# Kernel tuning notes

Measured on AMD Instinct MI355X. Metric: run time of the kernel, lower is better.

Reference implementation:

```python
import jax, jax.numpy as jnp
import numpy as np

EPS = 0.5          # residual scaling (module __init__ eps)
N = 100_000        # num nodes
E = 1_250_000      # num edges (avg degree ~12.5)
D = 64             # feature dim


def setup_inputs() -> dict:
    key = jax.random.key(0)
    k1, k2, k3 = jax.random.split(key, 3)
    x = jax.random.normal(k1, (N, D), dtype=jnp.float32)
    src = jax.random.randint(k2, (E,), 0, N, dtype=jnp.int32)
    dst = jax.random.randint(k3, (E,), 0, N, dtype=jnp.int32)
    return {"x": x, "src": src, "dst": dst}


def reference(x, src, dst):
    n = x.shape[0]
    # out-degree of each node = number of edges with that node as source
    deg = jax.ops.segment_sum(jnp.ones(src.shape, dtype=x.dtype), src, num_segments=n)
    norm = jnp.power(jnp.maximum(deg, 1.0), -0.5)          # [N]
    edge_norm = norm[src] * norm[dst]                      # [E] (u_mul_v)
    msg = x[src] * edge_norm[:, None]                      # [E, D] (u_mul_e)
    h = jax.ops.segment_sum(msg, dst, num_segments=n)      # sum per destination
    return h + x * EPS
```

## Files before the change

### kernel.cpp

```cpp
#include <hip/hip_runtime.h>

constexpr int D        = 64;
constexpr float EPS    = 0.5f;
constexpr int BKT      = 256;
constexpr int CAPB_MAX = 4096;
constexpr int EPB      = 4096;
constexpr int PTHREADS = 512;
constexpr int EPT      = EPB / PTHREADS;
constexpr int GTHREADS = 1024;
constexpr int NTHREADS = 512;
constexpr int NBMAX    = 512;
constexpr int MAXOVF   = 65536;

__device__ __forceinline__ unsigned int f2bf(float f) {
    unsigned int u = __float_as_uint(f);
    return (u + 0x7FFFu + ((u >> 16) & 1u)) >> 16;
}
__device__ __forceinline__ float bf2f_lo(unsigned int v) { return __uint_as_float(v << 16); }
__device__ __forceinline__ float bf2f_hi(unsigned int v) { return __uint_as_float(v & 0xFFFF0000u); }


__global__ __launch_bounds__(PTHREADS)
void partition_kernel(const int* __restrict__ src, const int* __restrict__ dst,
                      int* __restrict__ curD, int* __restrict__ curS,
                      unsigned int* __restrict__ rec, unsigned char* __restrict__ srec,
                      int* __restrict__ ovf_cnt, int* __restrict__ ovf,
                      int* __restrict__ sovf_cnt, int* __restrict__ sovf,
                      int E, int NB, int capb) {
    __shared__ int histD[NBMAX];
    __shared__ int histS[NBMAX];
    __shared__ int startD[NBMAX];
    __shared__ int startS[NBMAX];
    const int base = blockIdx.x * EPB;
    const int tid  = threadIdx.x;
    const bool full = (base + EPB) <= E;
    for (int b = tid; b < NB; b += PTHREADS) { histD[b] = 0; histS[b] = 0; }
    __syncthreads();

    if (full) {
        const int4* s4 = (const int4*)(src + base);
        const int4* d4 = (const int4*)(dst + base);
        #pragma unroll
        for (int k = 0; k < EPT / 4; ++k) {
            int4 sv = s4[tid + k * PTHREADS];
            int4 dv = d4[tid + k * PTHREADS];
            atomicAdd(&histD[dv.x >> 8], 1); atomicAdd(&histS[sv.x >> 8], 1);
            atomicAdd(&histD[dv.y >> 8], 1); atomicAdd(&histS[sv.y >> 8], 1);
            atomicAdd(&histD[dv.z >> 8], 1); atomicAdd(&histS[sv.z >> 8], 1);
            atomicAdd(&histD[dv.w >> 8], 1); atomicAdd(&histS[sv.w >> 8], 1);
        }
    } else {
        for (int k = 0; k < EPT; ++k) {
            int e = base + tid + k * PTHREADS;
            if (e < E) {
                atomicAdd(&histD[dst[e] >> 8], 1);
                atomicAdd(&histS[src[e] >> 8], 1);
            }
        }
    }
    __syncthreads();
    for (int b = tid; b < NB; b += PTHREADS) {
        int c = histD[b];
        startD[b] = (c > 0) ? atomicAdd(&curD[b], c) : 0;
        histD[b] = 0;
        int c2 = histS[b];
        startS[b] = (c2 > 0) ? atomicAdd(&curS[b], c2) : 0;
        histS[b] = 0;
    }
    __syncthreads();
    if (full) {
        const int4* s4 = (const int4*)(src + base);
        const int4* d4 = (const int4*)(dst + base);
        #pragma unroll
        for (int k = 0; k < EPT / 4; ++k) {
            int4 sv = s4[tid + k * PTHREADS];
            int4 dv = d4[tid + k * PTHREADS];
            int ss[4] = {sv.x, sv.y, sv.z, sv.w};
            int tt[4] = {dv.x, dv.y, dv.z, dv.w};
            #pragma unroll
            for (int j = 0; j < 4; ++j) {
                int s = ss[j], t = tt[j];
                int bD = t >> 8;
                int r  = atomicAdd(&histD[bD], 1);
                int p  = startD[bD] + r;
                if (p < capb) {
                    rec[(size_t)bD * capb + p] = ((unsigned int)s << 8) | (unsigned int)(t & (BKT - 1));
                } else {
                    int i = atomicAdd(ovf_cnt, 1);
                    if (i < MAXOVF) { ovf[2 * i] = s; ovf[2 * i + 1] = t; }
                }
                int bS = s >> 8;
                int r2 = atomicAdd(&histS[bS], 1);
                int p2 = startS[bS] + r2;
                if (p2 < capb) {
                    srec[(size_t)bS * capb + p2] = (unsigned char)(s & (BKT - 1));
                } else {
                    int i = atomicAdd(sovf_cnt, 1);
                    if (i < MAXOVF) sovf[i] = s;
                }
            }
        }
    } else {
        for (int k = 0; k < EPT; ++k) {
            int e = base + tid + k * PTHREADS;
            if (e < E) {
                int s = src[e], t = dst[e];
                int bD = t >> 8;
                int r  = atomicAdd(&histD[bD], 1);
                int p  = startD[bD] + r;
                if (p < capb) {
                    rec[(size_t)bD * capb + p] = ((unsigned int)s << 8) | (unsigned int)(t & (BKT - 1));
                } else {
                    int i = atomicAdd(ovf_cnt, 1);
                    if (i < MAXOVF) { ovf[2 * i] = s; ovf[2 * i + 1] = t; }
                }
                int bS = s >> 8;
                int r2 = atomicAdd(&histS[bS], 1);
                int p2 = startS[bS] + r2;
                if (p2 < capb) {
                    srec[(size_t)bS * capb + p2] = (unsigned char)(s & (BKT - 1));
                } else {
                    int i = atomicAdd(sovf_cnt, 1);
                    if (i < MAXOVF) sovf[i] = s;
                }
            }
        }
    }
}

__global__ __launch_bounds__(NTHREADS)
void degnorm_kernel(const unsigned char* __restrict__ srec, const int* __restrict__ curS,
                    const int* __restrict__ sovf_cnt, const int* __restrict__ sovf,
                    float* __restrict__ norm, int n, int capb) {
    const int b   = blockIdx.x;
    const int tid = threadIdx.x;
    __shared__ int hist[BKT];
    if (tid < BKT) hist[tid] = 0;
    __syncthreads();
    int cnt = curS[b];
    if (cnt > capb) cnt = capb;
    const unsigned int* s4 = (const unsigned int*)(srec + (size_t)b * capb);
    int nw = cnt >> 2;
    for (int i = tid; i < nw; i += NTHREADS) {
        unsigned int w = s4[i];
        atomicAdd(&hist[w & 255u], 1);
        atomicAdd(&hist[(w >> 8) & 255u], 1);
        atomicAdd(&hist[(w >> 16) & 255u], 1);
        atomicAdd(&hist[w >> 24], 1);
    }
    for (int i = (nw << 2) + tid; i < cnt; i += NTHREADS)
        atomicAdd(&hist[srec[(size_t)b * capb + i]], 1);
    int oc = *sovf_cnt;
    if (oc > 0) {
        if (oc > MAXOVF) oc = MAXOVF;
        for (int i = tid; i < oc; i += NTHREADS) {
            int s = sovf[i];
            if ((s >> 8) == b) atomicAdd(&hist[s & (BKT - 1)], 1);
        }
    }
    __syncthreads();
    if (tid < BKT) {
        int node = b * BKT + tid;
        if (node < n) norm[node] = rsqrtf(fmaxf((float)hist[tid], 1.0f));
    }
}

__global__ __launch_bounds__(256)
void yhconv_kernel(const float2* __restrict__ x2, const float* __restrict__ norm,
                   unsigned int* __restrict__ yh, int total) {
    int stride = gridDim.x * 256;
    for (int i = blockIdx.x * 256 + threadIdx.x; i < total; i += stride) {
        float2 v = x2[i];
        float nm = norm[i >> 5];
        yh[i] = f2bf(v.x * nm) | (f2bf(v.y * nm) << 16);
    }
}

__global__ __launch_bounds__(GTHREADS)
void sortgather_kernel(const unsigned int* __restrict__ rec, const int* __restrict__ curD,
                       const float* __restrict__ norm, const uint4* __restrict__ yr4,
                       const float4* __restrict__ x4, float4* __restrict__ out4,
                       int n, int capb) {
    __shared__ unsigned int recs[CAPB_MAX];
    __shared__ unsigned int srcs[CAPB_MAX];
    __shared__ int hist[BKT];
    __shared__ int rankb[BKT];
    __shared__ int rsL[BKT];
    __shared__ float nrmL[BKT];
    __shared__ unsigned int wsums[GTHREADS / 64];
    const int b   = blockIdx.x;
    const int tid = threadIdx.x;
    const int lane = tid & 63;
    const int wid  = tid >> 6;

    int cnt = curD[b];
    if (cnt > capb) cnt = capb;
    for (int i = tid; i < cnt; i += GTHREADS) recs[i] = rec[(size_t)b * capb + i];
    if (tid < BKT) {
        hist[tid] = 0;
        int node = b * BKT + tid;
        nrmL[tid] = (node < n) ? norm[node] : 1.0f;
    }
    __syncthreads();
    for (int i = tid; i < cnt; i += GTHREADS) atomicAdd(&hist[recs[i] & (BKT - 1)], 1);
    __syncthreads();
    {
        int v = (tid < BKT) ? hist[tid] : 0;
        #pragma unroll
        for (int off = 1; off < 64; off <<= 1) {
            int t = __shfl_up(v, off);
            if (lane >= off) v += t;
        }
        if (tid < BKT && lane == 63) wsums[wid] = (unsigned int)v;
        __syncthreads();
        if (tid < BKT) {
            int add = 0;
            #pragma unroll
            for (int w = 0; w < BKT / 64; ++w)
                if (w < wid) add += (int)wsums[w];
            int excl = v + add - hist[tid];
            rankb[tid] = excl;
            rsL[tid]   = excl;
        }
    }
    __syncthreads();
    for (int i = tid; i < cnt; i += GTHREADS) {
        unsigned int v = recs[i];
        int pos = atomicAdd(&rankb[v & (BKT - 1)], 1);
        srcs[pos] = v >> 8;
    }
    __syncthreads();

    const int fl  = lane & 7;
    const int oct = lane >> 3;
    #pragma unroll
    for (int r = 0; r < BKT / 128; ++r) {
        int ln   = r * 128 + wid * 8 + oct;
        int node = b * BKT + ln;
        bool valid = node < n;
        int rsl = valid ? rsL[ln]  : 0;
        int cl  = valid ? hist[ln] : 0;
        int m = cl;
        m = max(m, __shfl_xor(m, 8));
        m = max(m, __shfl_xor(m, 16));
        m = max(m, __shfl_xor(m, 32));
        float a0 = 0.f, a1 = 0.f, a2 = 0.f, a3 = 0.f;
        float a4 = 0.f, a5 = 0.f, a6 = 0.f, a7 = 0.f;
        for (int k = 0; k < m; k += 8) {
            int sb[8];
            #pragma unroll
            for (int j = 0; j < 8; ++j) {
                int kj = k + j;
                sb[j] = (kj < cl) ? (int)srcs[rsl + kj] : -1;
            }
            #pragma unroll
            for (int j = 0; j < 8; ++j) {
                bool take = sb[j] >= 0;
                int s = take ? sb[j] : 0;
                uint4 v = yr4[(size_t)s * 8 + fl];
                if (!take) { v.x = 0u; v.y = 0u; v.z = 0u; v.w = 0u; }
                a0 += bf2f_lo(v.x); a1 += bf2f_hi(v.x);
                a2 += bf2f_lo(v.y); a3 += bf2f_hi(v.y);
                a4 += bf2f_lo(v.z); a5 += bf2f_hi(v.z);
                a6 += bf2f_lo(v.w); a7 += bf2f_hi(v.w);
            }
        }
        if (valid) {
            float nt = nrmL[ln];
            size_t basei = (size_t)node * 16 + fl * 2;
            float4 xv0 = x4[basei], xv1 = x4[basei + 1];
            float4 r0, r1;
            r0.x = a0 * nt + EPS * xv0.x;  r0.y = a1 * nt + EPS * xv0.y;
            r0.z = a2 * nt + EPS * xv0.z;  r0.w = a3 * nt + EPS * xv0.w;
            r1.x = a4 * nt + EPS * xv1.x;  r1.y = a5 * nt + EPS * xv1.y;
            r1.z = a6 * nt + EPS * xv1.z;  r1.w = a7 * nt + EPS * xv1.w;
            out4[basei] = r0;
            out4[basei + 1] = r1;
        }
    }
}

__global__ void cleanup_kernel(const float* __restrict__ x, const float* __restrict__ norm,
                               const int* __restrict__ ovf_cnt, const int* __restrict__ ovf,
                               float* __restrict__ out) {
    int cnt = *ovf_cnt;
    if (cnt > MAXOVF) cnt = MAXOVF;
    long long total = (long long)cnt * D;
    long long stride = (long long)gridDim.x * blockDim.x;
    for (long long i = blockIdx.x * (long long)blockDim.x + threadIdx.x; i < total; i += stride) {
        int e = (int)(i >> 6), d = (int)(i & 63);
        int s = ovf[2 * e], t = ovf[2 * e + 1];
        atomicAdd(&out[(size_t)t * D + d], norm[s] * norm[t] * x[(size_t)s * D + d]);
    }
}


__global__ void fb_hist(const int* __restrict__ src, int* __restrict__ deg, int E) {
    int e = blockIdx.x * blockDim.x + threadIdx.x;
    if (e < E) atomicAdd(&deg[src[e]], 1);
}
__global__ void fb_norm(const int* __restrict__ deg, float* __restrict__ norm, int n) {
    int i = blockIdx.x * blockDim.x + threadIdx.x;
    if (i < n) norm[i] = rsqrtf(fmaxf((float)deg[i], 1.0f));
}
__global__ void fb_init_out(const float4* __restrict__ x, float4* __restrict__ out, int n4) {
    int i = blockIdx.x * blockDim.x + threadIdx.x;
    if (i < n4) {
        float4 v = x[i];
        out[i] = make_float4(v.x * EPS, v.y * EPS, v.z * EPS, v.w * EPS);
    }
}
__global__ void fb_scatter(const float* __restrict__ x, const int* __restrict__ src,
                           const int* __restrict__ dst, const float* __restrict__ norm,
                           float* __restrict__ out, int E) {
    long long tid = (long long)blockIdx.x * blockDim.x + threadIdx.x;
    int e = (int)(tid >> 6), d = (int)(tid & 63);
    if (e < E) {
        int s = src[e], t = dst[e];
        atomicAdd(&out[(size_t)t * D + d], norm[s] * norm[t] * x[(size_t)s * D + d]);
    }
}


extern "C" void kernel_launch(void* const* d_in, const int* in_sizes, int n_in,
                              void* d_out, int out_size, void* d_ws, size_t ws_size,
                              hipStream_t stream) {
    const float* x   = (const float*)d_in[0];
    const int*   src = (const int*)d_in[1];
    const int*   dst = (const int*)d_in[2];
    float* out = (float*)d_out;

    const int ND = in_sizes[0];
    const int E  = in_sizes[1];
    const int n  = ND / D;
    const int NB = (n + BKT - 1) / BKT;
    constexpr int B = 256;
    const int NB64 = (NB + 63) & ~63;

    int capb = 0;
    for (int c : {4096, 3584}) {
        size_t srecB = ((size_t)NB * c + 15) & ~15ull;
        size_t need = (size_t)NB * c * 4
                    + srecB
                    + (size_t)ND * 2
                    + (size_t)n * 4
                    + (size_t)(2 * NB64 + 128) * 4
                    + (size_t)3 * MAXOVF * 4;
        if (need <= ws_size) { capb = c; break; }
    }

    if (NB <= NBMAX && capb > 0 && n < (1 << 24) && E > 0) {
        unsigned int* rec   = (unsigned int*)d_ws;
        unsigned char* srec = (unsigned char*)(rec + (size_t)NB * capb);
        size_t srecB        = ((size_t)NB * capb + 15) & ~15ull;
        unsigned int* yh    = (unsigned int*)(srec + srecB);
        float* norm         = (float*)(yh + ND / 2);
        int* curD           = (int*)(norm + n);
        int* curS           = curD + NB64;
        int* ovf_cnt        = curS + NB64;
        int* sovf_cnt       = ovf_cnt + 64;
        int* ovf            = sovf_cnt + 64;
        int* sovf           = ovf + 2 * MAXOVF;

        hipMemsetAsync(curD, 0, (size_t)(2 * NB64 + 128) * 4, stream);
        partition_kernel<<<(E + EPB - 1) / EPB, PTHREADS, 0, stream>>>(src, dst, curD, curS,
                                                                       rec, srec, ovf_cnt, ovf,
                                                                       sovf_cnt, sovf, E, NB, capb);
        degnorm_kernel<<<NB, NTHREADS, 0, stream>>>(srec, curS, sovf_cnt, sovf, norm, n, capb);
        int yt = ND / 2;
        int yg = (yt + 255) / 256; if (yg > 2048) yg = 2048;
        yhconv_kernel<<<yg, B, 0, stream>>>((const float2*)x, norm, yh, yt);
        sortgather_kernel<<<NB, GTHREADS, 0, stream>>>(rec, curD, norm, (const uint4*)yh,
                                                       (const float4*)x, (float4*)out, n, capb);
        cleanup_kernel<<<32, B, 0, stream>>>(x, norm, ovf_cnt, ovf, out);
    } else {
        int*   deg  = (int*)d_ws;
        float* norm = (float*)d_ws + n;
        hipMemsetAsync(deg, 0, (size_t)n * sizeof(int), stream);
        fb_hist<<<(E + B - 1) / B, B, 0, stream>>>(src, deg, E);
        fb_norm<<<(n + B - 1) / B, B, 0, stream>>>(deg, norm, n);
        fb_init_out<<<(ND / 4 + B - 1) / B, B, 0, stream>>>((const float4*)x, (float4*)out, ND / 4);
        long long total = (long long)E * D;
        fb_scatter<<<(int)((total + B - 1) / B), B, 0, stream>>>(x, src, dst, norm, out, E);
    }
}
```

Before: 142.7 us.

## Split destination partition into two-pass radix scatter with LDS-sorted coalesced writes

Replaces the single-pass scatter of edges into 391 destination buckets with two passes. The first pass sorts each 8192-edge chunk into 13 coarse groups in shared memory and writes contiguous runs. The second pass re-sorts each group slice into 32 fine buckets in shared memory before writing. The goal is to turn scattered 4-byte global writes into coalesced runs. The cost is an extra kernel, an extra read and write of the edge records, and a larger workspace.

```diff
diff --git a/kernel.cpp b/kernel.cpp
--- a/kernel.cpp
+++ b/kernel.cpp
@@ -4,9 +4,12 @@
 constexpr float EPS    = 0.5f;
 constexpr int BKT      = 256;
 constexpr int CAPB_MAX = 4096;
-constexpr int EPB      = 4096;
+constexpr int GBITS    = 13;
+constexpr int GSZ      = 1 << GBITS;
+constexpr int NGMAX    = 64;
+constexpr int EPB1     = 8192;
+constexpr int SL2      = 4096;
 constexpr int PTHREADS = 512;
-constexpr int EPT      = EPB / PTHREADS;
 constexpr int GTHREADS = 1024;
 constexpr int NTHREADS = 512;
 constexpr int NBMAX    = 512;
@@ -19,50 +22,71 @@
 __device__ __forceinline__ float bf2f_lo(unsigned int v) { return __uint_as_float(v << 16); }
 __device__ __forceinline__ float bf2f_hi(unsigned int v) { return __uint_as_float(v & 0xFFFF0000u); }
 
+__device__ __forceinline__ int findseg(const int* lo, int nseg, int i) {
+    int a = 0, b = nseg;
+    while (b - a > 1) { int m = (a + b) >> 1; if (i >= lo[m]) a = m; else b = m; }
+    return a;
+}
+
 
 __global__ __launch_bounds__(PTHREADS)
-void partition_kernel(const int* __restrict__ src, const int* __restrict__ dst,
-                      int* __restrict__ curD, int* __restrict__ curS,
-                      unsigned int* __restrict__ rec, unsigned char* __restrict__ srec,
-                      int* __restrict__ ovf_cnt, int* __restrict__ ovf,
-                      int* __restrict__ sovf_cnt, int* __restrict__ sovf,
-                      int E, int NB, int capb) {
-    __shared__ int histD[NBMAX];
-    __shared__ int histS[NBMAX];
-    __shared__ int startD[NBMAX];
-    __shared__ int startS[NBMAX];
-    const int base = blockIdx.x * EPB;
+void pass1_kernel(const int* __restrict__ src, const int* __restrict__ dst,
+                  int* __restrict__ cur1, int* __restrict__ curS,
+                  unsigned int* __restrict__ rec1, unsigned char* __restrict__ srec,
+                  int* __restrict__ ovf_cnt, int* __restrict__ ovf,
+                  int* __restrict__ sovf_cnt, int* __restrict__ sovf,
+                  int E, int NB, int NG, int cap1, int capb) {
+    __shared__ unsigned int srt1[EPB1];
+    __shared__ int histG[NGMAX], startG[NGMAX], lo1[NGMAX + 1];
+    __shared__ int histS[NBMAX], startS[NBMAX];
+    const int base = blockIdx.x * EPB1;
     const int tid  = threadIdx.x;
-    const bool full = (base + EPB) <= E;
-    for (int b = tid; b < NB; b += PTHREADS) { histD[b] = 0; histS[b] = 0; }
+    const int lane = tid & 63;
+    const int cnt  = min(EPB1, E - base);
+    const bool full = (cnt == EPB1);
+
+    if (tid < NGMAX) histG[tid] = 0;
+    for (int b = tid; b < NB; b += PTHREADS) histS[b] = 0;
     __syncthreads();
 
     if (full) {
         const int4* s4 = (const int4*)(src + base);
         const int4* d4 = (const int4*)(dst + base);
         #pragma unroll
-        for (int k = 0; k < EPT / 4; ++k) {
+        for (int k = 0; k < EPB1 / PTHREADS / 4; ++k) {
             int4 sv = s4[tid + k * PTHREADS];
             int4 dv = d4[tid + k * PTHREADS];
-            atomicAdd(&histD[dv.x >> 8], 1); atomicAdd(&histS[sv.x >> 8], 1);
-            atomicAdd(&histD[dv.y >> 8], 1); atomicAdd(&histS[sv.y >> 8], 1);
-            atomicAdd(&histD[dv.z >> 8], 1); atomicAdd(&histS[sv.z >> 8], 1);
-            atomicAdd(&histD[dv.w >> 8], 1); atomicAdd(&histS[sv.w >> 8], 1);
+            atomicAdd(&histG[dv.x >> GBITS], 1); atomicAdd(&histS[sv.x >> 8], 1);
+            atomicAdd(&histG[dv.y >> GBITS], 1); atomicAdd(&histS[sv.y >> 8], 1);
+            atomicAdd(&histG[dv.z >> GBITS], 1); atomicAdd(&histS[sv.z >> 8], 1);
+            atomicAdd(&histG[dv.w >> GBITS], 1); atomicAdd(&histS[sv.w >> 8], 1);
         }
     } else {
-        for (int k = 0; k < EPT; ++k) {
-            int e = base + tid + k * PTHREADS;
-            if (e < E) {
-                atomicAdd(&histD[dst[e] >> 8], 1);
-                atomicAdd(&histS[src[e] >> 8], 1);
+        for (int k = 0; k < EPB1 / PTHREADS; ++k) {
+            int e = tid + k * PTHREADS;
+            if (e < cnt) {
+                atomicAdd(&histG[dst[base + e] >> GBITS], 1);
+                atomicAdd(&histS[src[base + e] >> 8], 1);
             }
         }
     }
     __syncthreads();
+    if (tid < 64) {
+        int orig = (tid < NG) ? histG[tid] : 0;
+        int v = orig;
+        #pragma unroll
+        for (int off = 1; off < 64; off <<= 1) {
+            int t = __shfl_up(v, off);
+            if (lane >= off) v += t;
+        }
+        if (tid < NG) {
+            lo1[tid] = v - orig;
+            if (tid == NG - 1) lo1[NG] = v;
+            startG[tid] = (orig > 0) ? atomicAdd(&cur1[tid], orig) : 0;
+            histG[tid] = 0;
+        }
+    }
     for (int b = tid; b < NB; b += PTHREADS) {
-        int c = histD[b];
-        startD[b] = (c > 0) ? atomicAdd(&curD[b], c) : 0;
-        histD[b] = 0;
         int c2 = histS[b];
         startS[b] = (c2 > 0) ? atomicAdd(&curS[b], c2) : 0;
         histS[b] = 0;
@@ -72,7 +96,7 @@
         const int4* s4 = (const int4*)(src + base);
         const int4* d4 = (const int4*)(dst + base);
         #pragma unroll
-        for (int k = 0; k < EPT / 4; ++k) {
+        for (int k = 0; k < EPB1 / PTHREADS / 4; ++k) {
             int4 sv = s4[tid + k * PTHREADS];
             int4 dv = d4[tid + k * PTHREADS];
             int ss[4] = {sv.x, sv.y, sv.z, sv.w};
@@ -80,20 +104,14 @@
             #pragma unroll
             for (int j = 0; j < 4; ++j) {
                 int s = ss[j], t = tt[j];
-                int bD = t >> 8;
-                int r  = atomicAdd(&histD[bD], 1);
-                int p  = startD[bD] + r;
-                if (p < capb) {
-                    rec[(size_t)bD * capb + p] = ((unsigned int)s << 8) | (unsigned int)(t & (BKT - 1));
-                } else {
-                    int i = atomicAdd(ovf_cnt, 1);
-                    if (i < MAXOVF) { ovf[2 * i] = s; ovf[2 * i + 1] = t; }
-                }
+                int g = t >> GBITS;
+                int r = atomicAdd(&histG[g], 1);
+                srt1[lo1[g] + r] = ((unsigned int)s << GBITS) | (unsigned int)(t & (GSZ - 1));
                 int bS = s >> 8;
                 int r2 = atomicAdd(&histS[bS], 1);
                 int p2 = startS[bS] + r2;
                 if (p2 < capb) {
-                    srec[(size_t)bS * capb + p2] = (unsigned char)(s & (BKT - 1));
+                    srec[(size_t)bS * capb + p2] = (unsigned char)(s & 255);
                 } else {
                     int i = atomicAdd(sovf_cnt, 1);
                     if (i < MAXOVF) sovf[i] = s;
@@ -101,29 +119,96 @@
             }
         }
     } else {
-        for (int k = 0; k < EPT; ++k) {
-            int e = base + tid + k * PTHREADS;
-            if (e < E) {
-                int s = src[e], t = dst[e];
-                int bD = t >> 8;
-                int r  = atomicAdd(&histD[bD], 1);
-                int p  = startD[bD] + r;
-                if (p < capb) {
-                    rec[(size_t)bD * capb + p] = ((unsigned int)s << 8) | (unsigned int)(t & (BKT - 1));
-                } else {
-                    int i = atomicAdd(ovf_cnt, 1);
-                    if (i < MAXOVF) { ovf[2 * i] = s; ovf[2 * i + 1] = t; }
-                }
+        for (int k = 0; k < EPB1 / PTHREADS; ++k) {
+            int e = tid + k * PTHREADS;
+            if (e < cnt) {
+                int s = src[base + e], t = dst[base + e];
+                int g = t >> GBITS;
+                int r = atomicAdd(&histG[g], 1);
+                srt1[lo1[g] + r] = ((unsigned int)s << GBITS) | (unsigned int)(t & (GSZ - 1));
                 int bS = s >> 8;
                 int r2 = atomicAdd(&histS[bS], 1);
                 int p2 = startS[bS] + r2;
                 if (p2 < capb) {
-                    srec[(size_t)bS * capb + p2] = (unsigned char)(s & (BKT - 1));
+                    srec[(size_t)bS * capb + p2] = (unsigned char)(s & 255);
                 } else {
                     int i = atomicAdd(sovf_cnt, 1);
                     if (i < MAXOVF) sovf[i] = s;
                 }
             }
+        }
+    }
+    __syncthreads();
+    for (int i = tid; i < cnt; i += PTHREADS) {
+        int g = findseg(lo1, NG, i);
+        int d = startG[g] + (i - lo1[g]);
+        unsigned int v = srt1[i];
+        if (d < cap1) {
+            rec1[(size_t)g * cap1 + d] = v;
+        } else {
+            int s = (int)(v >> GBITS);
+            int t = (g << GBITS) | (int)(v & (GSZ - 1));
+            int i2 = atomicAdd(ovf_cnt, 1);
+            if (i2 < MAXOVF) { ovf[2 * i2] = s; ovf[2 * i2 + 1] = t; }
+        }
+    }
+}
+
+__global__ __launch_bounds__(PTHREADS)
+void pass2_kernel(const unsigned int* __restrict__ rec1, const int* __restrict__ cur1,
+                  int* __restrict__ curD, unsigned int* __restrict__ rec,
+                  int* __restrict__ ovf_cnt, int* __restrict__ ovf,
+                  int NG, int SPG, int cap1, int capb) {
+    __shared__ unsigned int srt[SL2];
+    __shared__ int hist32[32], start32[32], lo32[33];
+    const int g   = blockIdx.x / SPG;
+    const int sl  = blockIdx.x % SPG;
+    const int tid = threadIdx.x;
+    const int lane = tid & 63;
+    int gcnt = cur1[g];
+    if (gcnt > cap1) gcnt = cap1;
+    const int base = sl * SL2;
+    const int cnt  = min(SL2, gcnt - base);
+    if (cnt <= 0) return;
+    const unsigned int* in = rec1 + (size_t)g * cap1 + base;
+
+    if (tid < 32) hist32[tid] = 0;
+    __syncthreads();
+    for (int i = tid; i < cnt; i += PTHREADS)
+        atomicAdd(&hist32[(in[i] & (GSZ - 1)) >> 8], 1);
+    __syncthreads();
+    if (tid < 32) {
+        int orig = hist32[tid];
+        int v = orig;
+        #pragma unroll
+        for (int off = 1; off < 32; off <<= 1) {
+            int t = __shfl_up(v, off);
+            if (lane >= off) v += t;
+        }
+        lo32[tid] = v - orig;
+        if (tid == 31) lo32[32] = v;
+        start32[tid] = (orig > 0) ? atomicAdd(&curD[g * 32 + tid], orig) : 0;
+        hist32[tid] = 0;
+    }
+    __syncthreads();
+    for (int i = tid; i < cnt; i += PTHREADS) {
+        unsigned int v = in[i];
+        int bg = (int)((v & (GSZ - 1)) >> 8);
+        int r  = atomicAdd(&hist32[bg], 1);
+        srt[lo32[bg] + r] = ((v >> GBITS) << 8) | (v & 255u);
+    }
+    __syncthreads();
+    for (int i = tid; i < cnt; i += PTHREADS) {
+        int bg = findseg(lo32, 32, i);
+        int d  = start32[bg] + (i - lo32[bg]);
+        unsigned int v = srt[i];
+        if (d < capb) {
+            rec[(size_t)(g * 32 + bg) * capb + d] = v;
+        } else {
+            int s = (int)(v >> 8);
+            int t = (g << GBITS) | (bg << 8) | (int)(v & 255u);
+            int i2 = atomicAdd(ovf_cnt, 1);
+            if (i2 < MAXOVF) { ovf[2 * i2] = s; ovf[2 * i2 + 1] = t; }
         }
     }
 }
@@ -155,7 +240,7 @@
         if (oc > MAXOVF) oc = MAXOVF;
         for (int i = tid; i < oc; i += NTHREADS) {
             int s = sovf[i];
-            if ((s >> 8) == b) atomicAdd(&hist[s & (BKT - 1)], 1);
+            if ((s >> 8) == b) atomicAdd(&hist[s & 255], 1);
         }
     }
     __syncthreads();
@@ -334,38 +419,49 @@
     const int E  = in_sizes[1];
     const int n  = ND / D;
     const int NB = (n + BKT - 1) / BKT;
+    const int NG = (n + GSZ - 1) >> GBITS;
     constexpr int B = 256;
     const int NB64 = (NB + 63) & ~63;
+    const int NG64 = 64;
+
+    const int cap1 = (((E + (NG > 0 ? NG : 1) - 1) / (NG > 0 ? NG : 1)) + 4096 + 15) & ~15;
+    const int SPG  = (cap1 + SL2 - 1) / SL2;
 
     int capb = 0;
     for (int c : {4096, 3584}) {
         size_t srecB = ((size_t)NB * c + 15) & ~15ull;
-        size_t need = (size_t)NB * c * 4
+        size_t need = (size_t)NG * cap1 * 4
+                    + (size_t)NB * c * 4
                     + srecB
                     + (size_t)ND * 2
                     + (size_t)n * 4
-                    + (size_t)(2 * NB64 + 128) * 4
+                    + (size_t)(NG64 + 2 * NB64 + 128) * 4
                     + (size_t)3 * MAXOVF * 4;
         if (need <= ws_size) { capb = c; break; }
     }
 
-    if (NB <= NBMAX && capb > 0 && n < (1 << 24) && E > 0) {
-        unsigned int* rec   = (unsigned int*)d_ws;
+    if (NB <= NBMAX && NG <= NGMAX && capb > 0 && n < (1 << 19) && E > 0) {
+        unsigned int* rec1  = (unsigned int*)d_ws;
+        unsigned int* rec   = rec1 + (size_t)NG * cap1;
         unsigned char* srec = (unsigned char*)(rec + (size_t)NB * capb);
         size_t srecB        = ((size_t)NB * capb + 15) & ~15ull;
         unsigned int* yh    = (unsigned int*)(srec + srecB);
         float* norm         = (float*)(yh + ND / 2);
-        int* curD           = (int*)(norm + n);
+        int* cur1           = (int*)(norm + n);
+        int* curD           = cur1 + NG64;
         int* curS           = curD + NB64;
         int* ovf_cnt        = curS + NB64;
         int* sovf_cnt       = ovf_cnt + 64;
         int* ovf            = sovf_cnt + 64;
         int* sovf           = ovf + 2 * MAXOVF;
 
-        hipMemsetAsync(curD, 0, (size_t)(2 * NB64 + 128) * 4, stream);
-        partition_kernel<<<(E + EPB - 1) / EPB, PTHREADS, 0, stream>>>(src, dst, curD, curS,
-                                                                       rec, srec, ovf_cnt, ovf,
-                                                                       sovf_cnt, sovf, E, NB, capb);
+        hipMemsetAsync(cur1, 0, (size_t)(NG64 + 2 * NB64 + 128) * 4, stream);
+        pass1_kernel<<<(E + EPB1 - 1) / EPB1, PTHREADS, 0, stream>>>(src, dst, cur1, curS,
+                                                                     rec1, srec, ovf_cnt, ovf,
+                                                                     sovf_cnt, sovf,
+                                                                     E, NB, NG, cap1, capb);
+        pass2_kernel<<<NG * SPG, PTHREADS, 0, stream>>>(rec1, cur1, curD, rec,
+                                                        ovf_cnt, ovf, NG, SPG, cap1, capb);
         degnorm_kernel<<<NB, NTHREADS, 0, stream>>>(srec, curS, sovf_cnt, sovf, norm, n, capb);
         int yt = ND / 2;
         int yg = (yt + 255) / 256; if (yg > 2048) yg = 2048;
```

After: 286.2 us. 2x slower.
